# Performance work log

Measured on AMD Instinct MI355X. Metric: run time of the kernel, lower is better.

The kernel has to match this reference:

```python
import jax, jax.numpy as jnp
import numpy as np

N_MET, N_RXN, D, C, H, E = 20000, 40000, 256, 64, 4, 250000
P = 0.2  # MC dropout prob (always active)


def setup_inputs() -> dict:
    key = jax.random.key(0)
    ks = jax.random.split(key, 40)
    g = lambda i, shape: jax.random.normal(ks[i], shape, jnp.float32) * 0.05
    inp = {
        'x_met': jax.random.normal(ks[0], (N_MET, D), jnp.float32),
        'x_rxn': jax.random.normal(ks[1], (N_RXN, D), jnp.float32),
        'sub_src': jax.random.randint(ks[2], (E,), 0, N_MET),
        'sub_dst': jax.random.randint(ks[3], (E,), 0, N_RXN),
        'prod_src': jax.random.randint(ks[4], (E,), 0, N_RXN),
        'prod_dst': jax.random.randint(ks[5], (E,), 0, N_MET),
        'shr_src': jax.random.randint(ks[6], (E,), 0, N_RXN),
        'shr_dst': jax.random.randint(ks[7], (E,), 0, N_RXN),
    }
    i = 8
    for name in ['sub', 'prod', 'shr']:
        inp['Wl_' + name] = g(i, (D, H * C)); inp['bl_' + name] = g(i + 1, (H * C,))
        inp['Wr_' + name] = g(i + 2, (D, H * C)); inp['br_' + name] = g(i + 3, (H * C,))
        inp['att_' + name] = g(i + 4, (H, C)); inp['b_' + name] = g(i + 5, (C,))
        i += 6
    inp['W_proj_rxn'] = g(26, (D, C)); inp['b_proj_rxn'] = g(27, (C,))
    inp['W_proj_met'] = g(28, (D, C)); inp['b_proj_met'] = g(29, (C,))
    inp['ln_rxn_g'] = jnp.ones((C,), jnp.float32); inp['ln_rxn_b'] = jnp.zeros((C,), jnp.float32)
    inp['ln_met_g'] = jnp.ones((C,), jnp.float32); inp['ln_met_b'] = jnp.zeros((C,), jnp.float32)
    return inp


def gatv2(xs, xd, src, dst, Wl, bl, Wr, br, att, bias, n_dst):
    # GATv2Conv (concat=False): mean over heads, eval-mode attention (no attn dropout).
    Hh, Cc = att.shape
    xl = (xs @ Wl + bl).reshape(xs.shape[0], Hh, Cc)  # source transform
    xr = (xd @ Wr + br).reshape(xd.shape[0], Hh, Cc)  # destination transform
    s = jax.nn.leaky_relu(xl[src] + xr[dst], 0.2)     # [E,H,C]
    e = jnp.einsum('ehc,hc->eh', s, att)              # [E,H] per-edge scores
    m = jax.ops.segment_max(e, dst, num_segments=n_dst)
    m = jnp.where(jnp.isfinite(m), m, 0.0)            # nodes with no in-edges
    ex = jnp.exp(e - m[dst])
    den = jax.ops.segment_sum(ex, dst, num_segments=n_dst)
    alpha = ex / (den[dst] + 1e-16)                   # segment softmax (PyG eps)
    out = jax.ops.segment_sum(alpha[:, :, None] * xl[src], dst, num_segments=n_dst)
    return out.mean(axis=1) + bias                    # [n_dst, C]


def layernorm(x, g, b):
    mu = x.mean(-1, keepdims=True)
    var = x.var(-1, keepdims=True)
    return (x - mu) * jax.lax.rsqrt(var + 1e-5) * g + b


def mc_dropout(x, key):
    mask = jax.random.bernoulli(key, 1.0 - P, x.shape)
    return jnp.where(mask, x / (1.0 - P), 0.0)


def reference(x_met, x_rxn, sub_src, sub_dst, prod_src, prod_dst, shr_src, shr_dst,
              Wl_sub, bl_sub, Wr_sub, br_sub, att_sub, b_sub,
              Wl_prod, bl_prod, Wr_prod, br_prod, att_prod, b_prod,
              Wl_shr, bl_shr, Wr_shr, br_shr, att_shr, b_shr,
              W_proj_rxn, b_proj_rxn, W_proj_met, b_proj_met,
              ln_rxn_g, ln_rxn_b, ln_met_g, ln_met_b):
    # shared_metabolite relation: add_self_loops=True
    sl = jnp.arange(N_RXN, dtype=shr_src.dtype)
    shr_src_f = jnp.concatenate([shr_src, sl])
    shr_dst_f = jnp.concatenate([shr_dst, sl])

    out_sub = gatv2(x_met, x_rxn, sub_src, sub_dst, Wl_sub, bl_sub, Wr_sub, br_sub, att_sub, b_sub, N_RXN)
    out_shr = gatv2(x_rxn, x_rxn, shr_src_f, shr_dst_f, Wl_shr, bl_shr, Wr_shr, br_shr, att_shr, b_shr, N_RXN)
    out_prod = gatv2(x_rxn, x_met, prod_src, prod_dst, Wl_prod, bl_prod, Wr_prod, br_prod, att_prod, b_prod, N_MET)

    rxn = 0.5 * (out_sub + out_shr)  # HeteroConv aggr='mean' over 2 relations
    met = out_prod                   # single relation -> mean is identity

    rxn = layernorm(jax.nn.elu(rxn) + (x_rxn @ W_proj_rxn + b_proj_rxn), ln_rxn_g, ln_rxn_b)
    met = layernorm(jax.nn.elu(met) + (x_met @ W_proj_met + b_proj_met), ln_met_g, ln_met_b)

    k1, k2 = jax.random.split(jax.random.key(1))
    return mc_dropout(rxn, k1), mc_dropout(met, k2)
```

## Files before the change

### kernel.cpp

```cpp
#include <hip/hip_runtime.h>
#include <hip/hip_bf16.h>
#include <stdint.h>

#define NMET 20000
#define NRXN 40000
#define DDIM 256
#define CDIM 64

typedef __attribute__((ext_vector_type(8))) short bf16x8;
typedef __attribute__((ext_vector_type(4))) float f32x4;

typedef __attribute__((address_space(1))) const void gvoid_t;
typedef __attribute__((address_space(3))) void lvoid_t;

__host__ __device__ inline void tf2x32(unsigned k0, unsigned k1,
                                       unsigned x0, unsigned x1,
                                       unsigned &o0, unsigned &o1) {
  unsigned ks2 = k0 ^ k1 ^ 0x1BD11BDAu;
#define TFR(r) { x0 += x1; x1 = (x1 << r) | (x1 >> (32 - r)); x1 ^= x0; }
  x0 += k0; x1 += k1;
  TFR(13) TFR(15) TFR(26) TFR(6)
  x0 += k1; x1 += ks2 + 1u;
  TFR(17) TFR(29) TFR(16) TFR(24)
  x0 += ks2; x1 += k0 + 2u;
  TFR(13) TFR(15) TFR(26) TFR(6)
  x0 += k0; x1 += k1 + 3u;
  TFR(17) TFR(29) TFR(16) TFR(24)
  x0 += k1; x1 += ks2 + 4u;
  TFR(13) TFR(15) TFR(26) TFR(6)
  x0 += ks2; x1 += k0 + 5u;
#undef TFR
  o0 = x0; o1 = x1;
}

__device__ inline unsigned short f2bbits(float f) {
  __hip_bfloat16 h = __float2bfloat16(f);
  return *reinterpret_cast<unsigned short*>(&h);
}
__device__ inline float b2f(unsigned short u) {
  unsigned v = (unsigned)u << 16;
  return __uint_as_float(v);
}

#define CVT_A_BLK 2500
#define CVT_B_BLK 5000
__global__ __launch_bounds__(256) void prep_all(
    const float* __restrict__ x_met, __hip_bfloat16* __restrict__ xmb,
    const float* __restrict__ x_rxn, __hip_bfloat16* __restrict__ xrb,
    const float* w0, const float* w1, const float* w2, const float* w3,
    const float* w4, const float* w5, const float* w6, const float* w7,
    __hip_bfloat16* o0, __hip_bfloat16* o1, __hip_bfloat16* o2, __hip_bfloat16* o3,
    __hip_bfloat16* o4, __hip_bfloat16* o5, __hip_bfloat16* o6, __hip_bfloat16* o7) {
  __shared__ float ts[32][33];
  int bid = blockIdx.x;
  if (bid < CVT_A_BLK + CVT_B_BLK) {
    const float* in; __hip_bfloat16* out; int n;
    if (bid < CVT_A_BLK) { in = x_met; out = xmb; n = NMET * DDIM; }
    else { in = x_rxn; out = xrb; n = NRXN * DDIM; bid -= CVT_A_BLK; }
    int i = (bid * 256 + threadIdx.x) * 8;
    if (i >= n) return;
    float4 va = *reinterpret_cast<const float4*>(in + i);
    float4 vb = *reinterpret_cast<const float4*>(in + i + 4);
    bf16x8 o;
    o[0] = (short)f2bbits(va.x); o[1] = (short)f2bbits(va.y);
    o[2] = (short)f2bbits(va.z); o[3] = (short)f2bbits(va.w);
    o[4] = (short)f2bbits(vb.x); o[5] = (short)f2bbits(vb.y);
    o[6] = (short)f2bbits(vb.z); o[7] = (short)f2bbits(vb.w);
    *reinterpret_cast<bf16x8*>(out + i) = o;
    return;
  }
  int t = bid - (CVT_A_BLK + CVT_B_BLK);
  int z = t >> 6, tt = t & 63;
  const float* w; __hip_bfloat16* o; int Ncols;
  switch (z) {
    case 0: w = w0; o = o0; Ncols = 256; break;
    case 1: w = w1; o = o1; Ncols = 256; break;
    case 2: w = w2; o = o2; Ncols = 256; break;
    case 3: w = w3; o = o3; Ncols = 256; break;
    case 4: w = w4; o = o4; Ncols = 256; break;
    case 5: w = w5; o = o5; Ncols = 256; break;
    case 6: w = w6; o = o6; Ncols = 64; break;
    default: w = w7; o = o7; Ncols = 64; break;
  }
  int ntile = Ncols / 32;
  if (tt >= ntile * 8) return;
  int tn = tt % ntile, tk = tt / ntile;
  int tx = threadIdx.x & 31, ty = threadIdx.x >> 5;
#pragma unroll
  for (int r = ty; r < 32; r += 8)
    ts[r][tx] = w[(size_t)(tk * 32 + r) * Ncols + tn * 32 + tx];
  __syncthreads();
#pragma unroll
  for (int r = ty; r < 32; r += 8)
    o[(size_t)(tn * 32 + r) * 256 + tk * 32 + tx] = __float2bfloat16(ts[tx][r]);
}

struct TDesc {
  const __hip_bfloat16* X;
  const __hip_bfloat16* W;
  const float* bias;
  __hip_bfloat16* Yb;
  float* Yf;
  int M, N, nt, blocks;
};
struct TD8 { TDesc g[8]; };

__global__ __launch_bounds__(256) void gemm_tiled8(TD8 gd, int ng) {
  __shared__ __align__(16) char As[16384];
  __shared__ __align__(16) char Bs[16384];
  int bid = blockIdx.x;
  int di = 0;
  while (di < ng && bid >= gd.g[di].blocks) { bid -= gd.g[di].blocks; ++di; }
  if (di >= ng) return;
  TDesc g = gd.g[di];
  int mrow = bid / g.nt, ntile = bid - mrow * g.nt;
  int m0 = mrow * 128, n0 = ntile * 128;
  int tid = threadIdx.x, wave = tid >> 6, lane = tid & 63;
  int lr = lane & 15, lk = lane >> 4;
  int wm = wave >> 1, wn = wave & 1;
  int brows = g.N - n0; if (brows > 128) brows = 128;
  int bch = brows >> 3;
  int lrow = lane >> 3;
  int gsw = ((lane & 7) ^ lrow) * 8;

  f32x4 acc[4][4] = {};
  for (int kt = 0; kt < 4; ++kt) {
    for (int c = wave; c < 16; c += 4) {
      int row = m0 + c * 8 + lrow;
      if (row > g.M - 1) row = g.M - 1;
      const void* src = g.X + (size_t)row * DDIM + kt * 64 + gsw;
      __builtin_amdgcn_global_load_lds((gvoid_t*)src, (lvoid_t*)(As + c * 1024), 16, 0, 0);
    }
    for (int c = wave; c < bch; c += 4) {
      int row = n0 + c * 8 + lrow;
      const void* src = g.W + (size_t)row * DDIM + kt * 64 + gsw;
      __builtin_amdgcn_global_load_lds((gvoid_t*)src, (lvoid_t*)(Bs + c * 1024), 16, 0, 0);
    }
    __syncthreads();
#pragma unroll
    for (int kk = 0; kk < 2; ++kk) {
      bf16x8 a[4], b[4];
#pragma unroll
      for (int m = 0; m < 4; ++m) {
        int row = wm * 64 + m * 16 + lr;
        int grp = (kk * 4 + lk) ^ (lr & 7);
        a[m] = *reinterpret_cast<const bf16x8*>(As + row * 128 + grp * 16);
      }
#pragma unroll
      for (int n = 0; n < 4; ++n) {
        int row = wn * 64 + n * 16 + lr;
        int grp = (kk * 4 + lk) ^ (lr & 7);
        b[n] = *reinterpret_cast<const bf16x8*>(Bs + row * 128 + grp * 16);
      }
#pragma unroll
      for (int m = 0; m < 4; ++m)
#pragma unroll
        for (int n = 0; n < 4; ++n)
          acc[m][n] = __builtin_amdgcn_mfma_f32_16x16x32_bf16(a[m], b[n], acc[m][n], 0, 0, 0);
    }
    __syncthreads();
  }
  bool isb = (g.Yb != nullptr);
#pragma unroll
  for (int m = 0; m < 4; ++m) {
#pragma unroll
    for (int rr = 0; rr < 4; ++rr) {
      int row = m0 + wm * 64 + m * 16 + lk * 4 + rr;
      if (row >= g.M) continue;
#pragma unroll
      for (int n = 0; n < 4; ++n) {
        int cg = n0 + wn * 64 + n * 16 + lr;
        if (cg >= g.N) continue;
        float v = acc[m][n][rr] + g.bias[cg];
        if (isb) g.Yb[(size_t)row * g.N + cg] = __float2bfloat16(v);
        else     g.Yf[(size_t)row * g.N + cg] = v;
      }
    }
  }
}

__global__ __launch_bounds__(256) void hist3(
    const int* __restrict__ d0, const int* __restrict__ d1, const int* __restrict__ d2,
    int E, int* __restrict__ c0, int* __restrict__ c1, int* __restrict__ c2) {
  int i = blockIdx.x * 256 + threadIdx.x;
  if (i >= E) return;
  int rel = blockIdx.y;
  if (rel == 0) atomicAdd(&c0[d0[i]], 1);
  else if (rel == 1) atomicAdd(&c1[d1[i]], 1);
  else atomicAdd(&c2[d2[i]], 1);
}

__global__ __launch_bounds__(256) void alloc3(
    const int* __restrict__ c0, const int* __restrict__ c1, const int* __restrict__ c2,
    int* __restrict__ o0, int* __restrict__ o1, int* __restrict__ o2,
    int* __restrict__ u0, int* __restrict__ u1, int* __restrict__ u2,
    int* __restrict__ cursors, int n0, int n1, int n2) {
  int rel = blockIdx.y;
  int i = blockIdx.x * 256 + threadIdx.x;
  const int* c = (rel == 0) ? c0 : (rel == 1) ? c1 : c2;
  int* o = (rel == 0) ? o0 : (rel == 1) ? o1 : o2;
  int* u = (rel == 0) ? u0 : (rel == 1) ? u1 : u2;
  int n = (rel == 0) ? n0 : (rel == 1) ? n1 : n2;
  if (i >= n) return;
  int cc = c[i];
  int pos = atomicAdd(&cursors[rel], cc);
  o[i] = pos; u[i] = pos;
}

__global__ __launch_bounds__(256) void scatter3(
    const int* __restrict__ s0, const int* __restrict__ d0,
    const int* __restrict__ s1, const int* __restrict__ d1,
    const int* __restrict__ s2, const int* __restrict__ d2,
    int E, int* __restrict__ u0, int* __restrict__ u1, int* __restrict__ u2,
    int* __restrict__ e0, int* __restrict__ e1, int* __restrict__ e2) {
  int i = blockIdx.x * 256 + threadIdx.x;
  if (i >= E) return;
  int rel = blockIdx.y;
  if (rel == 0)      { int pos = atomicAdd(&u0[d0[i]], 1); e0[pos] = s0[i]; }
  else if (rel == 1) { int pos = atomicAdd(&u1[d1[i]], 1); e1[pos] = s1[i]; }
  else               { int pos = atomicAdd(&u2[d2[i]], 1); e2[pos] = s2[i]; }
}

struct GatRel {
  const __hip_bfloat16* xl;
  const __hip_bfloat16* xr;
  const int* off; const int* cnt; const int* srce;
  const float* att; float* acc;
  int n; int self_loop;
};

__global__ __launch_bounds__(256) void gat3(GatRel r0, GatRel r1, GatRel r2) {
  int gidx = blockIdx.x * 4 + (threadIdx.x >> 6);
  int lane = threadIdx.x & 63;
  GatRel r; int d;
  if (gidx < r0.n) { r = r0; d = gidx; }
  else if (gidx < r0.n + r1.n) { r = r1; d = gidx - r0.n; }
  else if (gidx < r0.n + r1.n + r2.n) { r = r2; d = gidx - r0.n - r1.n; }
  else return;

  ushort4 ur = *reinterpret_cast<const ushort4*>(r.xr + (size_t)d * DDIM + 4 * lane);
  float c0 = b2f(ur.x), c1 = b2f(ur.y), c2 = b2f(ur.z), c3 = b2f(ur.w);
  float4 at = *reinterpret_cast<const float4*>(r.att + 4 * lane);

  float den = 0.f;
  float a0 = 0.f, a1 = 0.f, a2 = 0.f, a3 = 0.f;

#define EDGE(s_) {                                                              \
    ushort4 ux = *reinterpret_cast<const ushort4*>(                             \
        r.xl + (size_t)(s_) * DDIM + 4 * lane);                                 \
    float x0 = b2f(ux.x), x1 = b2f(ux.y), x2 = b2f(ux.z), x3 = b2f(ux.w);       \
    float t0 = x0 + c0; t0 = (t0 >= 0.f) ? t0 : 0.2f * t0;                      \
    float t1 = x1 + c1; t1 = (t1 >= 0.f) ? t1 : 0.2f * t1;                      \
    float t2 = x2 + c2; t2 = (t2 >= 0.f) ? t2 : 0.2f * t2;                      \
    float t3 = x3 + c3; t3 = (t3 >= 0.f) ? t3 : 0.2f * t3;                      \
    float pp = t0 * at.x + t1 * at.y + t2 * at.z + t3 * at.w;                   \
    pp += __shfl_xor(pp, 1); pp += __shfl_xor(pp, 2);                           \
    pp += __shfl_xor(pp, 4); pp += __shfl_xor(pp, 8);                           \
    float ex = __expf(pp);                                                      \
    den += ex;                                                                  \
    a0 = fmaf(ex, x0, a0); a1 = fmaf(ex, x1, a1);                               \
    a2 = fmaf(ex, x2, a2); a3 = fmaf(ex, x3, a3);                               \
  }

  if (r.self_loop) EDGE(d);
  int cnt = r.cnt[d];
  int beg = r.off[d];
  for (int jb = 0; jb < cnt; jb += 64) {
    int jj = jb + lane; if (jj > cnt - 1) jj = cnt - 1;
    int srcv = r.srce[beg + jj];
    int lim = cnt - jb; if (lim > 64) lim = 64;
    for (int u = 0; u < lim; ++u) {
      int s = __shfl(srcv, u);
      EDGE(s);
    }
  }
#undef EDGE

  float inv = (den > 0.f) ? 1.0f / den : 0.f;
  float p0 = a0 * inv, p1 = a1 * inv, p2 = a2 * inv, p3 = a3 * inv;
  p0 += __shfl_xor(p0, 16); p0 += __shfl_xor(p0, 32);
  p1 += __shfl_xor(p1, 16); p1 += __shfl_xor(p1, 32);
  p2 += __shfl_xor(p2, 16); p2 += __shfl_xor(p2, 32);
  p3 += __shfl_xor(p3, 16); p3 += __shfl_xor(p3, 32);
  int srcl = lane >> 2;
  float v0 = __shfl(p0, srcl);
  float v1 = __shfl(p1, srcl);
  float v2 = __shfl(p2, srcl);
  float v3 = __shfl(p3, srcl);
  float val = (lane & 2) ? ((lane & 1) ? v3 : v2) : ((lane & 1) ? v1 : v0);
  r.acc[(size_t)d * 64 + lane] = 0.25f * val;
}

struct FDesc {
  const float* accA; const float* accB;
  float* out;
  const float* bA; const float* bB; float scale;
  const float* g; const float* be;
  int n; unsigned key0, key1;
};

__global__ __launch_bounds__(256) void finalize2(FDesc f0, FDesc f1) {
  int gidx = blockIdx.x * 4 + (threadIdx.x >> 6);
  int lane = threadIdx.x & 63;
  FDesc f; int d;
  if (gidx < f0.n) { f = f0; d = gidx; }
  else if (gidx < f0.n + f1.n) { f = f1; d = gidx - f0.n; }
  else return;
  unsigned idx = (unsigned)d * 64u + (unsigned)lane;
  float bias = f.bA[lane] + (f.bB ? f.bB[lane] : 0.f);
  float agg = f.accA[idx] + (f.accB ? f.accB[idx] : 0.f);
  float pre = f.scale * (agg + bias);
  pre = (pre > 0.f) ? pre : expm1f(pre);
  pre += f.out[idx];
  float mu = pre;
#pragma unroll
  for (int off = 32; off; off >>= 1) mu += __shfl_xor(mu, off);
  mu *= (1.0f / 64.0f);
  float dv = pre - mu;
  float var = dv * dv;
#pragma unroll
  for (int off = 32; off; off >>= 1) var += __shfl_xor(var, off);
  var *= (1.0f / 64.0f);
  float y = dv * rsqrtf(var + 1e-5f) * f.g[lane] + f.be[lane];
  unsigned o0, o1;
  tf2x32(f.key0, f.key1, 0u, idx, o0, o1);
  unsigned bits = o0 ^ o1;
  float u = __uint_as_float((bits >> 9) | 0x3f800000u) - 1.0f;
  y = (u < 0.8f) ? y / 0.8f : 0.0f;
  f.out[idx] = y;
}

extern "C" void kernel_launch(void* const* d_in, const int* in_sizes, int n_in,
                              void* d_out, int out_size, void* d_ws, size_t ws_size,
                              hipStream_t stream) {
  const float* x_met = (const float*)d_in[0];
  const float* x_rxn = (const float*)d_in[1];
  const int* sub_src = (const int*)d_in[2];
  const int* sub_dst = (const int*)d_in[3];
  const int* prod_src = (const int*)d_in[4];
  const int* prod_dst = (const int*)d_in[5];
  const int* shr_src = (const int*)d_in[6];
  const int* shr_dst = (const int*)d_in[7];
  const float* Wl_sub = (const float*)d_in[8];
  const float* bl_sub = (const float*)d_in[9];
  const float* Wr_sub = (const float*)d_in[10];
  const float* br_sub = (const float*)d_in[11];
  const float* att_sub = (const float*)d_in[12];
  const float* b_sub = (const float*)d_in[13];
  const float* Wl_prod = (const float*)d_in[14];
  const float* bl_prod = (const float*)d_in[15];
  const float* Wr_prod = (const float*)d_in[16];
  const float* br_prod = (const float*)d_in[17];
  const float* att_prod = (const float*)d_in[18];
  const float* b_prod = (const float*)d_in[19];
  const float* Wl_shr = (const float*)d_in[20];
  const float* bl_shr = (const float*)d_in[21];
  const float* Wr_shr = (const float*)d_in[22];
  const float* br_shr = (const float*)d_in[23];
  const float* att_shr = (const float*)d_in[24];
  const float* b_shr = (const float*)d_in[25];
  const float* W_proj_rxn = (const float*)d_in[26];
  const float* b_proj_rxn = (const float*)d_in[27];
  const float* W_proj_met = (const float*)d_in[28];
  const float* b_proj_met = (const float*)d_in[29];
  const float* ln_rxn_g = (const float*)d_in[30];
  const float* ln_rxn_b = (const float*)d_in[31];
  const float* ln_met_g = (const float*)d_in[32];
  const float* ln_met_b = (const float*)d_in[33];

  const int E = in_sizes[2];

  char* p = (char*)d_ws;
  auto take = [&](size_t b) { char* q = p; p += (b + 255) & ~(size_t)255; return q; };
  __hip_bfloat16* xmb = (__hip_bfloat16*)take((size_t)NMET * DDIM * 2);
  __hip_bfloat16* xrb = (__hip_bfloat16*)take((size_t)NRXN * DDIM * 2);
  __hip_bfloat16* wt[8];
  for (int i = 0; i < 6; ++i) wt[i] = (__hip_bfloat16*)take(256 * 256 * 2);
  for (int i = 6; i < 8; ++i) wt[i] = (__hip_bfloat16*)take(64 * 256 * 2);
  float* acc_sub = (float*)take((size_t)NRXN * CDIM * 4);
  float* acc_shr = (float*)take((size_t)NRXN * CDIM * 4);
  float* acc_met = (float*)take((size_t)NMET * CDIM * 4);
  int* cnt_sub = (int*)take((size_t)NRXN * 4 + (size_t)NRXN * 4 + (size_t)NMET * 4 + 16);
  int* cnt_shr = cnt_sub + NRXN;
  int* cnt_prod = cnt_shr + NRXN;
  int* cursors = cnt_prod + NMET;
  int* off_sub = (int*)take((size_t)NRXN * 4);
  int* off_shr = (int*)take((size_t)NRXN * 4);
  int* off_prod = (int*)take((size_t)NMET * 4);
  int* cur_sub = (int*)take((size_t)NRXN * 4);
  int* cur_shr = (int*)take((size_t)NRXN * 4);
  int* cur_prod = (int*)take((size_t)NMET * 4);
  int* srce_sub = (int*)take((size_t)E * 4);
  int* srce_shr = (int*)take((size_t)E * 4);
  int* srce_prod = (int*)take((size_t)E * 4);

  size_t met_b = (size_t)NMET * DDIM * 2, rxn_b = (size_t)NRXN * DDIM * 2;
  size_t used = (size_t)(p - (char*)d_ws);
  bool big = (ws_size >= used + 3 * met_b + 3 * rxn_b + 4096);

  __hip_bfloat16 *xl_sub, *xr_sub, *xl_shr, *xr_shr, *xl_prod, *xr_prod;
  if (big) {
    xl_sub = (__hip_bfloat16*)take(met_b);
    xr_sub = (__hip_bfloat16*)take(rxn_b);
    xl_shr = (__hip_bfloat16*)take(rxn_b);
    xr_shr = (__hip_bfloat16*)take(rxn_b);
    xl_prod = (__hip_bfloat16*)take(rxn_b);
    xr_prod = (__hip_bfloat16*)take(met_b);
  } else {
    __hip_bfloat16* xa = (__hip_bfloat16*)take(rxn_b);
    __hip_bfloat16* xb = (__hip_bfloat16*)take(rxn_b);
    xl_sub = xl_shr = xl_prod = xa;
    xr_sub = xr_shr = xr_prod = xb;
  }

  float* out_rxn = (float*)d_out;
  float* out_met = out_rxn + (size_t)NRXN * CDIM;

  unsigned k1_0, k1_1, k2_0, k2_1;
  tf2x32(0u, 1u, 0u, 0u, k1_0, k1_1);
  tf2x32(0u, 1u, 0u, 1u, k2_0, k2_1);

  dim3 blk(256);

  hipMemsetAsync(cnt_sub, 0, ((size_t)(NRXN + NRXN + NMET) + 4) * 4, stream);
  hist3<<<dim3((E + 255) / 256, 3), blk, 0, stream>>>(
      sub_dst, shr_dst, prod_dst, E, cnt_sub, cnt_shr, cnt_prod);
  alloc3<<<dim3((NRXN + 255) / 256, 3), blk, 0, stream>>>(
      cnt_sub, cnt_shr, cnt_prod, off_sub, off_shr, off_prod,
      cur_sub, cur_shr, cur_prod, cursors, NRXN, NRXN, NMET);
  prep_all<<<CVT_A_BLK + CVT_B_BLK + 512, blk, 0, stream>>>(
      x_met, xmb, x_rxn, xrb,
      Wl_sub, Wr_sub, Wl_shr, Wr_shr, Wl_prod, Wr_prod, W_proj_rxn, W_proj_met,
      wt[0], wt[1], wt[2], wt[3], wt[4], wt[5], wt[6], wt[7]);
  scatter3<<<dim3((E + 255) / 256, 3), blk, 0, stream>>>(
      sub_src, sub_dst, shr_src, shr_dst, prod_src, prod_dst, E,
      cur_sub, cur_shr, cur_prod, srce_sub, srce_shr, srce_prod);

  auto mk = [](const __hip_bfloat16* X, const __hip_bfloat16* W, const float* bias,
               __hip_bfloat16* Yb, float* Yf, int M, int N) {
    TDesc g; g.X = X; g.W = W; g.bias = bias; g.Yb = Yb; g.Yf = Yf;
    g.M = M; g.N = N; g.nt = (N + 127) / 128;
    g.blocks = ((M + 127) / 128) * g.nt;
    return g;
  };
  auto mkrel = [](const __hip_bfloat16* xl, const __hip_bfloat16* xr,
                  const int* off, const int* cnt, const int* srce,
                  const float* att, float* acc, int n, int sl) {
    GatRel r; r.xl = xl; r.xr = xr; r.off = off; r.cnt = cnt; r.srce = srce;
    r.att = att; r.acc = acc; r.n = n; r.self_loop = sl;
    return r;
  };
  GatRel rz{}; rz.n = 0;

  TDesc dsub_r  = mk(xrb, wt[1], br_sub,     xr_sub,  nullptr, NRXN, DDIM);
  TDesc dshr_l  = mk(xrb, wt[2], bl_shr,     xl_shr,  nullptr, NRXN, DDIM);
  TDesc dshr_r  = mk(xrb, wt[3], br_shr,     xr_shr,  nullptr, NRXN, DDIM);
  TDesc dprod_l = mk(xrb, wt[4], bl_prod,    xl_prod, nullptr, NRXN, DDIM);
  TDesc dproj_r = mk(xrb, wt[6], b_proj_rxn, nullptr, out_rxn, NRXN, CDIM);
  TDesc dsub_l  = mk(xmb, wt[0], bl_sub,     xl_sub,  nullptr, NMET, DDIM);
  TDesc dprod_m = mk(xmb, wt[5], br_prod,    xr_prod, nullptr, NMET, DDIM);
  TDesc dproj_m = mk(xmb, wt[7], b_proj_met, nullptr, out_met, NMET, CDIM);

  GatRel rsub = mkrel(xl_sub, xr_sub, off_sub, cnt_sub, srce_sub, att_sub, acc_sub, NRXN, 0);
  GatRel rshr = mkrel(xl_shr, xr_shr, off_shr, cnt_shr, srce_shr, att_shr, acc_shr, NRXN, 1);
  GatRel rprod = mkrel(xl_prod, xr_prod, off_prod, cnt_prod, srce_prod, att_prod, acc_met, NMET, 0);

  if (big) {
    TD8 gd = {{dsub_r, dshr_l, dshr_r, dprod_l, dproj_r, dsub_l, dprod_m, dproj_m}};
    int tot = 0;
    for (int i = 0; i < 8; ++i) tot += gd.g[i].blocks;
    gemm_tiled8<<<tot, blk, 0, stream>>>(gd, 8);
    gat3<<<(NRXN + NRXN + NMET + 3) / 4, blk, 0, stream>>>(rsub, rshr, rprod);
  } else {
    TD8 gd1 = {{dproj_r, dproj_m, dsub_l, dsub_r}};
    int t1 = gd1.g[0].blocks + gd1.g[1].blocks + gd1.g[2].blocks + gd1.g[3].blocks;
    gemm_tiled8<<<t1, blk, 0, stream>>>(gd1, 4);
    gat3<<<(NRXN + 3) / 4, blk, 0, stream>>>(rsub, rz, rz);
    TD8 gd2 = {{dshr_l, dshr_r}};
    int t2 = gd2.g[0].blocks + gd2.g[1].blocks;
    gemm_tiled8<<<t2, blk, 0, stream>>>(gd2, 2);
    gat3<<<(NRXN + 3) / 4, blk, 0, stream>>>(rshr, rz, rz);
    TD8 gd3 = {{dprod_l, dprod_m}};
    int t3 = gd3.g[0].blocks + gd3.g[1].blocks;
    gemm_tiled8<<<t3, blk, 0, stream>>>(gd3, 2);
    gat3<<<(NMET + 3) / 4, blk, 0, stream>>>(rprod, rz, rz);
  }

  FDesc f0, f1;
  f0.accA = acc_sub; f0.accB = acc_shr; f0.out = out_rxn;
  f0.bA = b_sub; f0.bB = b_shr; f0.scale = 0.5f;
  f0.g = ln_rxn_g; f0.be = ln_rxn_b; f0.n = NRXN; f0.key0 = k1_0; f0.key1 = k1_1;
  f1.accA = acc_met; f1.accB = nullptr; f1.out = out_met;
  f1.bA = b_prod; f1.bB = nullptr; f1.scale = 1.0f;
  f1.g = ln_met_g; f1.be = ln_met_b; f1.n = NMET; f1.key0 = k2_0; f1.key1 = k2_1;
  finalize2<<<(NRXN + NMET + 3) / 4, blk, 0, stream>>>(f0, f1);
}
```

Baseline: 336.3 us.

## Double-buffer GEMM LDS tiles and batch GAT edge gathers four at a time

The GEMM kernel gets two LDS buffers per operand and issues the global-to-LDS loads for the next K tile while the MFMAs run on the current one, so load latency overlaps compute. The GAT aggregation loop now issues four independent row gathers before processing them, giving more loads in flight per wave. Leaky-ReLU uses fmaxf instead of a select. Doubling LDS to 64KB per block may reduce occupancy. The diff never shows the loop-end __syncthreads being removed, so whether the GEMM synchronisation is still correct cannot be checked from the visible code.

```diff
diff --git a/kernel.cpp b/kernel.cpp
--- a/kernel.cpp
+++ b/kernel.cpp
@@ -106,8 +106,8 @@
 struct TD8 { TDesc g[8]; };
 
 __global__ __launch_bounds__(256) void gemm_tiled8(TD8 gd, int ng) {
-  __shared__ __align__(16) char As[16384];
-  __shared__ __align__(16) char Bs[16384];
+  __shared__ __align__(16) char As[2][16384];
+  __shared__ __align__(16) char Bs[2][16384];
   int bid = blockIdx.x;
   int di = 0;
   while (di < ng && bid >= gd.g[di].blocks) { bid -= gd.g[di].blocks; ++di; }
@@ -123,20 +123,27 @@
   int lrow = lane >> 3;
   int gsw = ((lane & 7) ^ lrow) * 8;
 
-  f32x4 acc[4][4] = {};
-  for (int kt = 0; kt < 4; ++kt) {
+  auto stage = [&](int buf, int kt) {
     for (int c = wave; c < 16; c += 4) {
       int row = m0 + c * 8 + lrow;
       if (row > g.M - 1) row = g.M - 1;
       const void* src = g.X + (size_t)row * DDIM + kt * 64 + gsw;
-      __builtin_amdgcn_global_load_lds((gvoid_t*)src, (lvoid_t*)(As + c * 1024), 16, 0, 0);
+      __builtin_amdgcn_global_load_lds((gvoid_t*)src, (lvoid_t*)(As[buf] + c * 1024), 16, 0, 0);
     }
     for (int c = wave; c < bch; c += 4) {
       int row = n0 + c * 8 + lrow;
       const void* src = g.W + (size_t)row * DDIM + kt * 64 + gsw;
-      __builtin_amdgcn_global_load_lds((gvoid_t*)src, (lvoid_t*)(Bs + c * 1024), 16, 0, 0);
+      __builtin_amdgcn_global_load_lds((gvoid_t*)src, (lvoid_t*)(Bs[buf] + c * 1024), 16, 0, 0);
     }
-    __syncthreads();
+  };
+
+  f32x4 acc[4][4] = {};
+  stage(0, 0);
+  __syncthreads();
+#pragma unroll
+  for (int kt = 0; kt < 4; ++kt) {
+    int cur = kt & 1;
+    if (kt < 3) stage(cur ^ 1, kt + 1);
 #pragma unroll
     for (int kk = 0; kk < 2; ++kk) {
       bf16x8 a[4], b[4];
@@ -144,13 +151,13 @@
       for (int m = 0; m < 4; ++m) {
         int row = wm * 64 + m * 16 + lr;
         int grp = (kk * 4 + lk) ^ (lr & 7);
-        a[m] = *reinterpret_cast<const bf16x8*>(As + row * 128 + grp * 16);
+        a[m] = *reinterpret_cast<const bf16x8*>(As[cur] + row * 128 + grp * 16);
       }
 #pragma unroll
       for (int n = 0; n < 4; ++n) {
         int row = wn * 64 + n * 16 + lr;
         int grp = (kk * 4 + lk) ^ (lr & 7);
-        b[n] = *reinterpret_cast<const bf16x8*>(Bs + row * 128 + grp * 16);
+        b[n] = *reinterpret_cast<const bf16x8*>(Bs[cur] + row * 128 + grp * 16);
       }
 #pragma unroll
       for (int m = 0; m < 4; ++m)
@@ -245,14 +252,12 @@
   float den = 0.f;
   float a0 = 0.f, a1 = 0.f, a2 = 0.f, a3 = 0.f;
 
-#define EDGE(s_) {                                                              \
-    ushort4 ux = *reinterpret_cast<const ushort4*>(                             \
-        r.xl + (size_t)(s_) * DDIM + 4 * lane);                                 \
+#define EBODY(ux) {                                                             \
     float x0 = b2f(ux.x), x1 = b2f(ux.y), x2 = b2f(ux.z), x3 = b2f(ux.w);       \
-    float t0 = x0 + c0; t0 = (t0 >= 0.f) ? t0 : 0.2f * t0;                      \
-    float t1 = x1 + c1; t1 = (t1 >= 0.f) ? t1 : 0.2f * t1;                      \
-    float t2 = x2 + c2; t2 = (t2 >= 0.f) ? t2 : 0.2f * t2;                      \
-    float t3 = x3 + c3; t3 = (t3 >= 0.f) ? t3 : 0.2f * t3;                      \
+    float t0 = x0 + c0; t0 = fmaxf(t0, 0.2f * t0);                              \
+    float t1 = x1 + c1; t1 = fmaxf(t1, 0.2f * t1);                              \
+    float t2 = x2 + c2; t2 = fmaxf(t2, 0.2f * t2);                              \
+    float t3 = x3 + c3; t3 = fmaxf(t3, 0.2f * t3);                              \
     float pp = t0 * at.x + t1 * at.y + t2 * at.z + t3 * at.w;                   \
     pp += __shfl_xor(pp, 1); pp += __shfl_xor(pp, 2);                           \
     pp += __shfl_xor(pp, 4); pp += __shfl_xor(pp, 8);                           \
@@ -261,20 +266,30 @@
     a0 = fmaf(ex, x0, a0); a1 = fmaf(ex, x1, a1);                               \
     a2 = fmaf(ex, x2, a2); a3 = fmaf(ex, x3, a3);                               \
   }
-
-  if (r.self_loop) EDGE(d);
+#define ELOAD(s_) *reinterpret_cast<const ushort4*>(r.xl + (size_t)(s_) * DDIM + 4 * lane)
+
+  if (r.self_loop) { ushort4 ux = ELOAD(d); EBODY(ux) }
   int cnt = r.cnt[d];
   int beg = r.off[d];
   for (int jb = 0; jb < cnt; jb += 64) {
     int jj = jb + lane; if (jj > cnt - 1) jj = cnt - 1;
     int srcv = r.srce[beg + jj];
     int lim = cnt - jb; if (lim > 64) lim = 64;
-    for (int u = 0; u < lim; ++u) {
+    int u = 0;
+    for (; u + 4 <= lim; u += 4) {
+      int s0 = __shfl(srcv, u), s1 = __shfl(srcv, u + 1);
+      int s2 = __shfl(srcv, u + 2), s3 = __shfl(srcv, u + 3);
+      ushort4 ux0 = ELOAD(s0); ushort4 ux1 = ELOAD(s1);
+      ushort4 ux2 = ELOAD(s2); ushort4 ux3 = ELOAD(s3);
+      EBODY(ux0) EBODY(ux1) EBODY(ux2) EBODY(ux3)
+    }
+    for (; u < lim; ++u) {
       int s = __shfl(srcv, u);
-      EDGE(s);
+      ushort4 ux = ELOAD(s); EBODY(ux)
     }
   }
-#undef EDGE
+#undef EBODY
+#undef ELOAD
 
   float inv = (den > 0.f) ? 1.0f / den : 0.f;
   float p0 = a0 * inv, p1 = a1 * inv, p2 = a2 * inv, p3 = a3 * inv;
```

New measurement: 370.1 us. 10.0% more time.

## Split each GAT destination node across two waves and unroll edge gathers by four

Applied to the files above, without the earlier changes.

The GAT aggregation kernel now gives each destination node two wavefronts, each covering two heads with two features per lane, and combines the head means through shared memory. The edge loop is unrolled by four so four gathered source rows are in flight before compute. The aim is more memory-level parallelism and occupancy on the latency-bound random gathers. In exchange it adds a block-wide barrier, a shared-memory combine, duplicated index loads and shuffles, and narrower 4-byte loads per lane.

```diff
diff --git a/kernel.cpp b/kernel.cpp
--- a/kernel.cpp
+++ b/kernel.cpp
@@ -230,65 +230,82 @@
 };
 
 __global__ __launch_bounds__(256) void gat3(GatRel r0, GatRel r1, GatRel r2) {
-  int gidx = blockIdx.x * 4 + (threadIdx.x >> 6);
+  __shared__ float2 comb[2][2][32];
+  int wave = threadIdx.x >> 6;
   int lane = threadIdx.x & 63;
-  GatRel r; int d;
-  if (gidx < r0.n) { r = r0; d = gidx; }
-  else if (gidx < r0.n + r1.n) { r = r1; d = gidx - r0.n; }
-  else if (gidx < r0.n + r1.n + r2.n) { r = r2; d = gidx - r0.n - r1.n; }
-  else return;
-
-  ushort4 ur = *reinterpret_cast<const ushort4*>(r.xr + (size_t)d * DDIM + 4 * lane);
-  float c0 = b2f(ur.x), c1 = b2f(ur.y), c2 = b2f(ur.z), c3 = b2f(ur.w);
-  float4 at = *reinterpret_cast<const float4*>(r.att + 4 * lane);
-
-  float den = 0.f;
-  float a0 = 0.f, a1 = 0.f, a2 = 0.f, a3 = 0.f;
-
-#define EDGE(s_) {                                                              \
-    ushort4 ux = *reinterpret_cast<const ushort4*>(                             \
-        r.xl + (size_t)(s_) * DDIM + 4 * lane);                                 \
-    float x0 = b2f(ux.x), x1 = b2f(ux.y), x2 = b2f(ux.z), x3 = b2f(ux.w);       \
-    float t0 = x0 + c0; t0 = (t0 >= 0.f) ? t0 : 0.2f * t0;                      \
-    float t1 = x1 + c1; t1 = (t1 >= 0.f) ? t1 : 0.2f * t1;                      \
-    float t2 = x2 + c2; t2 = (t2 >= 0.f) ? t2 : 0.2f * t2;                      \
-    float t3 = x3 + c3; t3 = (t3 >= 0.f) ? t3 : 0.2f * t3;                      \
-    float pp = t0 * at.x + t1 * at.y + t2 * at.z + t3 * at.w;                   \
-    pp += __shfl_xor(pp, 1); pp += __shfl_xor(pp, 2);                           \
-    pp += __shfl_xor(pp, 4); pp += __shfl_xor(pp, 8);                           \
-    float ex = __expf(pp);                                                      \
-    den += ex;                                                                  \
-    a0 = fmaf(ex, x0, a0); a1 = fmaf(ex, x1, a1);                               \
-    a2 = fmaf(ex, x2, a2); a3 = fmaf(ex, x3, a3);                               \
-  }
-
-  if (r.self_loop) EDGE(d);
-  int cnt = r.cnt[d];
-  int beg = r.off[d];
-  for (int jb = 0; jb < cnt; jb += 64) {
-    int jj = jb + lane; if (jj > cnt - 1) jj = cnt - 1;
-    int srcv = r.srce[beg + jj];
-    int lim = cnt - jb; if (lim > 64) lim = 64;
-    for (int u = 0; u < lim; ++u) {
-      int s = __shfl(srcv, u);
-      EDGE(s);
+  int slot = wave >> 1;
+  int hh = wave & 1;
+  int gidx = blockIdx.x * 2 + slot;
+  int tot = r0.n + r1.n + r2.n;
+  bool valid = (gidx < tot);
+
+  GatRel r; int d = 0;
+  if (valid) {
+    if (gidx < r0.n) { r = r0; d = gidx; }
+    else if (gidx < r0.n + r1.n) { r = r1; d = gidx - r0.n; }
+    else { r = r2; d = gidx - r0.n - r1.n; }
+  }
+
+  float y0 = 0.f, y1 = 0.f;
+  if (valid) {
+    int h = hh * 2 + (lane >> 5);
+    int foff = h * 64 + (lane & 31) * 2;
+    ushort2 ur = *reinterpret_cast<const ushort2*>(r.xr + (size_t)d * DDIM + foff);
+    float c0v = b2f(ur.x), c1v = b2f(ur.y);
+    float2 at = *reinterpret_cast<const float2*>(r.att + foff);
+
+    float den = 0.f, a0 = 0.f, a1 = 0.f;
+
+#define EBODY(ux) {                                                             \
+      float x0 = b2f(ux.x), x1 = b2f(ux.y);                                     \
+      float t0 = x0 + c0v; t0 = fmaxf(t0, 0.2f * t0);                           \
+      float t1 = x1 + c1v; t1 = fmaxf(t1, 0.2f * t1);                           \
+      float pp = t0 * at.x + t1 * at.y;                                         \
+      pp += __shfl_xor(pp, 1); pp += __shfl_xor(pp, 2);                         \
+      pp += __shfl_xor(pp, 4); pp += __shfl_xor(pp, 8);                         \
+      pp += __shfl_xor(pp, 16);                                                 \
+      float ex = __expf(pp);                                                    \
+      den += ex;                                                                \
+      a0 = fmaf(ex, x0, a0); a1 = fmaf(ex, x1, a1);                             \
     }
-  }
-#undef EDGE
-
-  float inv = (den > 0.f) ? 1.0f / den : 0.f;
-  float p0 = a0 * inv, p1 = a1 * inv, p2 = a2 * inv, p3 = a3 * inv;
-  p0 += __shfl_xor(p0, 16); p0 += __shfl_xor(p0, 32);
-  p1 += __shfl_xor(p1, 16); p1 += __shfl_xor(p1, 32);
-  p2 += __shfl_xor(p2, 16); p2 += __shfl_xor(p2, 32);
-  p3 += __shfl_xor(p3, 16); p3 += __shfl_xor(p3, 32);
-  int srcl = lane >> 2;
-  float v0 = __shfl(p0, srcl);
-  float v1 = __shfl(p1, srcl);
-  float v2 = __shfl(p2, srcl);
-  float v3 = __shfl(p3, srcl);
-  float val = (lane & 2) ? ((lane & 1) ? v3 : v2) : ((lane & 1) ? v1 : v0);
-  r.acc[(size_t)d * 64 + lane] = 0.25f * val;
+#define ELOAD(s_) *reinterpret_cast<const ushort2*>(r.xl + (size_t)(s_) * DDIM + foff)
+
+    if (r.self_loop) { ushort2 ux = ELOAD(d); EBODY(ux) }
+    int cnt = r.cnt[d];
+    int beg = r.off[d];
+    for (int jb = 0; jb < cnt; jb += 64) {
+      int jj = jb + lane; if (jj > cnt - 1) jj = cnt - 1;
+      int srcv = r.srce[beg + jj];
+      int lim = cnt - jb; if (lim > 64) lim = 64;
+      int u = 0;
+      for (; u + 4 <= lim; u += 4) {
+        int s0 = __shfl(srcv, u), s1 = __shfl(srcv, u + 1);
+        int s2 = __shfl(srcv, u + 2), s3 = __shfl(srcv, u + 3);
+        ushort2 ux0 = ELOAD(s0); ushort2 ux1 = ELOAD(s1);
+        ushort2 ux2 = ELOAD(s2); ushort2 ux3 = ELOAD(s3);
+        EBODY(ux0) EBODY(ux1) EBODY(ux2) EBODY(ux3)
+      }
+      for (; u < lim; ++u) {
+        int s = __shfl(srcv, u);
+        ushort2 ux = ELOAD(s); EBODY(ux)
+      }
+    }
+#undef EBODY
+#undef ELOAD
+
+    float inv = (den > 0.f) ? 1.0f / den : 0.f;
+    y0 = a0 * inv; y1 = a1 * inv;
+    y0 += __shfl_xor(y0, 32);
+    y1 += __shfl_xor(y1, 32);
+    if (lane < 32) comb[slot][hh][lane] = make_float2(y0, y1);
+  }
+  __syncthreads();
+  if (valid && hh == 0 && lane < 32) {
+    float2 A = comb[slot][0][lane];
+    float2 B = comb[slot][1][lane];
+    float2 o; o.x = 0.25f * (A.x + B.x); o.y = 0.25f * (A.y + B.y);
+    *reinterpret_cast<float2*>(r.acc + (size_t)d * 64 + lane * 2) = o;
+  }
 }
 
 struct FDesc {
@@ -470,20 +487,20 @@
     int tot = 0;
     for (int i = 0; i < 8; ++i) tot += gd.g[i].blocks;
     gemm_tiled8<<<tot, blk, 0, stream>>>(gd, 8);
-    gat3<<<(NRXN + NRXN + NMET + 3) / 4, blk, 0, stream>>>(rsub, rshr, rprod);
+    gat3<<<(NRXN + NRXN + NMET + 1) / 2, blk, 0, stream>>>(rsub, rshr, rprod);
   } else {
     TD8 gd1 = {{dproj_r, dproj_m, dsub_l, dsub_r}};
     int t1 = gd1.g[0].blocks + gd1.g[1].blocks + gd1.g[2].blocks + gd1.g[3].blocks;
     gemm_tiled8<<<t1, blk, 0, stream>>>(gd1, 4);
-    gat3<<<(NRXN + 3) / 4, blk, 0, stream>>>(rsub, rz, rz);
+    gat3<<<(NRXN + 1) / 2, blk, 0, stream>>>(rsub, rz, rz);
     TD8 gd2 = {{dshr_l, dshr_r}};
     int t2 = gd2.g[0].blocks + gd2.g[1].blocks;
     gemm_tiled8<<<t2, blk, 0, stream>>>(gd2, 2);
-    gat3<<<(NRXN + 3) / 4, blk, 0, stream>>>(rshr, rz, rz);
+    gat3<<<(NRXN + 1) / 2, blk, 0, stream>>>(rshr, rz, rz);
     TD8 gd3 = {{dprod_l, dprod_m}};
     int t3 = gd3.g[0].blocks + gd3.g[1].blocks;
     gemm_tiled8<<<t3, blk, 0, stream>>>(gd3, 2);
-    gat3<<<(NMET + 3) / 4, blk, 0, stream>>>(rprod, rz, rz);
+    gat3<<<(NMET + 1) / 2, blk, 0, stream>>>(rprod, rz, rz);
   }
 
   FDesc f0, f1;
```

Result: slower. 364.9 us (+8.5%).
